# Optimization experiments

Measured on AMD Instinct MI355X. Metric: run time of the kernel, lower is better.

## Reference

```python
import jax, jax.numpy as jnp
import numpy as np


def setup_inputs() -> dict:
    key = jax.random.key(0)
    k1, k2, k3 = jax.random.split(key, 3)
    B, Cin, Cout, L, K = 16, 64, 64, 65536, 3
    return {
        "x": jax.random.normal(k1, (B, Cin, L), dtype=jnp.float32),
        "alpha": jnp.zeros((1, Cin, 1), dtype=jnp.float32),
        "weight": jax.random.normal(k2, (Cout, Cin, K), dtype=jnp.float32),
        "weight_scale": jnp.ones((Cout, 1, 1), dtype=jnp.float32),
        "bias": jax.random.normal(k3, (Cout,), dtype=jnp.float32),
        "beta": jnp.ones((1, Cout, 1), dtype=jnp.float32),
        "gamma": jnp.zeros((1, Cout, 1), dtype=jnp.float32),
        "zeta": jnp.zeros((1, Cout, 1), dtype=jnp.float32),
    }


def _rsign(x, alpha):
    # forward: sign(x - alpha) in {-1,+1}; backward: identity w.r.t. x (STE)
    signed = jnp.where(x >= alpha, 1.0, -1.0).astype(x.dtype)
    return x + jax.lax.stop_gradient(signed - x)


def _clipped_ste_sign(w):
    # forward: sign(w); backward: grad passes only where |w| <= 1 (Bi-RealNet)
    w_bin = jnp.sign(w)
    mask = (jnp.abs(w) <= 1.0).astype(w.dtype)
    wm = w * mask
    return jax.lax.stop_gradient(w_bin) + wm - jax.lax.stop_gradient(wm)


def _rprelu(x, beta, gamma, zeta):
    xs = x - gamma
    return jnp.where(x > gamma, xs + zeta, beta * xs + zeta)


def reference(x, alpha, weight, weight_scale, bias, beta, gamma, zeta):
    # RSign -> scaled binary conv1d (stride=1, pad=1) -> RPReLU
    xb = _rsign(x, alpha)                        # [B,Cin,L], values +-1
    wb = _clipped_ste_sign(weight) * weight_scale  # [Cout,Cin,K]
    y = jax.lax.conv_general_dilated(
        xb, wb, window_strides=(1,), padding=[(1, 1)],
        dimension_numbers=("NCH", "OIH", "NCH"))  # [B,Cout,L]
    y = y + bias[None, :, None]
    return _rprelu(y, beta, gamma, zeta)
```

## Files before the change

kernel.cpp:

```cpp
#include <hip/hip_runtime.h>

#define LLEN 65536
#define CIN 64
#define COUT 64
#define BROW (LLEN + 8)

typedef float f32x4 __attribute__((ext_vector_type(4)));
typedef unsigned long long u64;
typedef u64 u64x4 __attribute__((ext_vector_type(4)));

struct __align__(64) WRec {
    u64 p0, p1, p2;
    float A;
    float S;
    float Bv, G, Z;
    float f0, f2;
    float pad[3];
};

__global__ void pack_weights(const float* __restrict__ w,
                             const float* __restrict__ wscale,
                             const float* __restrict__ bias,
                             const float* __restrict__ beta,
                             const float* __restrict__ gamma,
                             const float* __restrict__ zeta,
                             WRec* __restrict__ rec) {
    int co = threadIdx.x;
    if (co >= COUT) return;
    const float* wr = w + co * (CIN * 3);
    u64 p[3] = {0, 0, 0}, nzw[3] = {0, 0, 0};
    #pragma unroll
    for (int q = 0; q < 4; ++q) {
        f32x4 buf[12];
        #pragma unroll
        for (int j = 0; j < 12; ++j)
            buf[j] = *(const f32x4*)(wr + q * 48 + 4 * j);
        #pragma unroll
        for (int j = 0; j < 12; ++j) {
            #pragma unroll
            for (int m = 0; m < 4; ++m) {
                const int idx = q * 48 + 4 * j + m;
                const int ci = idx / 3, k = idx % 3;
                const float wv = buf[j][m];
                p[k]   |= ((u64)(wv > 0.0f)) << ci;
                nzw[k] |= ((u64)(wv != 0.0f)) << ci;
            }
        }
    }
    const int n0 = __popcll(nzw[0]), n1 = __popcll(nzw[1]), n2 = __popcll(nzw[2]);
    WRec r;
    float s = wscale[co];
    r.p0 = p[0]; r.p1 = p[1]; r.p2 = p[2];
    r.A  = s * (float)(n0 + n1 + n2) + bias[co];
    r.S  = -2.0f * s;
    r.Bv = beta[co]; r.G = gamma[co]; r.Z = zeta[co];
    r.f0 = 0.5f * (float)n0;
    r.f2 = 0.5f * (float)n2;
    r.pad[0] = r.pad[1] = r.pad[2] = 0.0f;
    rec[co] = r;
}

__global__ void __launch_bounds__(256) pack_x(
        const float* __restrict__ x,
        const float* __restrict__ alpha,
        u64* __restrict__ bits) {
    const int t = threadIdx.x;
    const int b = blockIdx.y;
    const int l0 = blockIdx.x * 1024 + 4 * t;
    const float* xb = x + (size_t)b * CIN * LLEN + l0;

    u64 w0 = 0, w1 = 0, w2 = 0, w3 = 0;
    #pragma unroll
    for (int q = 0; q < 8; ++q) {
        f32x4 buf[8];
        #pragma unroll
        for (int j = 0; j < 8; ++j)
            buf[j] = *(const f32x4*)(xb + (size_t)(q * 8 + j) * LLEN);
        #pragma unroll
        for (int j = 0; j < 8; ++j) {
            const int ci = q * 8 + j;
            const float a = alpha[ci];
            w0 |= ((u64)(buf[j].x >= a)) << ci;
            w1 |= ((u64)(buf[j].y >= a)) << ci;
            w2 |= ((u64)(buf[j].z >= a)) << ci;
            w3 |= ((u64)(buf[j].w >= a)) << ci;
        }
    }
    u64x4 v; v.x = w0; v.y = w1; v.z = w2; v.w = w3;
    *(u64x4*)(bits + (size_t)b * BROW + l0 + 4) = v;
}

__device__ __forceinline__ float rprelu(float y, float B, float G, float Z) {
    float xs = y - G;
    return (y > G) ? (xs + Z) : fmaf(B, xs, Z);
}

__global__ void __launch_bounds__(256) bconv_compute(
        const u64* __restrict__ bits,
        const WRec* __restrict__ rec,
        float* __restrict__ out) {
    const int t     = threadIdx.x;
    const int co    = blockIdx.x;
    const int chunk = blockIdx.y;
    const int b     = blockIdx.z;
    const int c0    = chunk * 8192;

    const WRec r = rec[co];
    const u64* base = bits + (size_t)b * BROW + c0 + 4 * t;
    float* outp = out + ((size_t)b * COUT + co) * LLEN + c0 + 4 * t;

    const bool lo = (chunk == 0) && (t == 0);
    const bool hi = (chunk == 7) && (t == 255);

    #pragma unroll 4
    for (int j = 0; j < 8; ++j) {
        const u64* src = base + 1024 * j;
        const u64 xq0 = src[3], xq1 = src[4], xq2 = src[5],
                  xq3 = src[6], xq4 = src[7], xq5 = src[8];

        float fx = (float)(__popcll(xq0 ^ r.p0) + __popcll(xq1 ^ r.p1)
                         + __popcll(xq2 ^ r.p2));
        float fy = (float)(__popcll(xq1 ^ r.p0) + __popcll(xq2 ^ r.p1)
                         + __popcll(xq3 ^ r.p2));
        float fz = (float)(__popcll(xq2 ^ r.p0) + __popcll(xq3 ^ r.p1)
                         + __popcll(xq4 ^ r.p2));
        float fw = (float)(__popcll(xq3 ^ r.p0) + __popcll(xq4 ^ r.p1)
                         + __popcll(xq5 ^ r.p2));
        if (j == 0 && lo)
            fx = (float)(__popcll(xq1 ^ r.p1) + __popcll(xq2 ^ r.p2)) + r.f0;
        if (j == 7 && hi)
            fw = (float)(__popcll(xq3 ^ r.p0) + __popcll(xq4 ^ r.p1)) + r.f2;

        f32x4 o;
        o.x = rprelu(fmaf(r.S, fx, r.A), r.Bv, r.G, r.Z);
        o.y = rprelu(fmaf(r.S, fy, r.A), r.Bv, r.G, r.Z);
        o.z = rprelu(fmaf(r.S, fz, r.A), r.Bv, r.G, r.Z);
        o.w = rprelu(fmaf(r.S, fw, r.A), r.Bv, r.G, r.Z);
        __builtin_nontemporal_store(o, (f32x4*)(outp + 1024 * j));
    }
}

extern "C" void kernel_launch(void* const* d_in, const int* in_sizes, int n_in,
                              void* d_out, int out_size, void* d_ws, size_t ws_size,
                              hipStream_t stream) {
    const float* x      = (const float*)d_in[0];
    const float* alpha  = (const float*)d_in[1];
    const float* w      = (const float*)d_in[2];
    const float* wscale = (const float*)d_in[3];
    const float* bias   = (const float*)d_in[4];
    const float* beta   = (const float*)d_in[5];
    const float* gamma  = (const float*)d_in[6];
    const float* zeta   = (const float*)d_in[7];
    float* out = (float*)d_out;

    WRec* rec = (WRec*)d_ws;
    u64* bits = (u64*)((char*)d_ws + 4096);

    pack_weights<<<1, 64, 0, stream>>>(w, wscale, bias, beta, gamma, zeta, rec);

    dim3 gridA(LLEN / 1024, 16);
    pack_x<<<gridA, 256, 0, stream>>>(x, alpha, bits);

    dim3 gridB(COUT, 8, 16);
    bconv_compute<<<gridB, 256, 0, stream>>>(bits, rec, out);
}
```

Before: 103.6 us.

## Fold weight packing into pack_x, double per-thread work, swap compute grid order

Removes the separate one-block weight-packing launch by running it from an extra column of blocks in pack_x. Each pack_x thread now handles two 4-element groups with nontemporal loads, halving the block count and raising memory-level parallelism. The compute grid now has the chunk as the fastest block index instead of the output channel, which changes which blocks run concurrently and how bit-packed input rows are reused in cache. Risks include higher register pressure in pack_x and worse L2 reuse of the packed bits across output channels.

```diff
diff --git a/kernel.cpp b/kernel.cpp
--- a/kernel.cpp
+++ b/kernel.cpp
@@ -4,6 +4,7 @@
 #define CIN 64
 #define COUT 64
 #define BROW (LLEN + 8)
+#define NBLK_A (LLEN / 2048)
 
 typedef float f32x4 __attribute__((ext_vector_type(4)));
 typedef unsigned long long u64;
@@ -18,13 +19,11 @@
     float pad[3];
 };
 
-__global__ void pack_weights(const float* __restrict__ w,
-                             const float* __restrict__ wscale,
-                             const float* __restrict__ bias,
-                             const float* __restrict__ beta,
-                             const float* __restrict__ gamma,
-                             const float* __restrict__ zeta,
-                             WRec* __restrict__ rec) {
+__device__ __forceinline__ void pack_weights_body(
+        const float* __restrict__ w, const float* __restrict__ wscale,
+        const float* __restrict__ bias, const float* __restrict__ beta,
+        const float* __restrict__ gamma, const float* __restrict__ zeta,
+        WRec* __restrict__ rec) {
     int co = threadIdx.x;
     if (co >= COUT) return;
     const float* wr = w + co * (CIN * 3);
@@ -63,31 +62,54 @@
 __global__ void __launch_bounds__(256) pack_x(
         const float* __restrict__ x,
         const float* __restrict__ alpha,
-        u64* __restrict__ bits) {
+        u64* __restrict__ bits,
+        const float* __restrict__ w,
+        const float* __restrict__ wscale,
+        const float* __restrict__ bias,
+        const float* __restrict__ beta,
+        const float* __restrict__ gamma,
+        const float* __restrict__ zeta,
+        WRec* __restrict__ rec) {
+    if (blockIdx.x == NBLK_A) {
+        if (blockIdx.y == 0)
+            pack_weights_body(w, wscale, bias, beta, gamma, zeta, rec);
+        return;
+    }
     const int t = threadIdx.x;
     const int b = blockIdx.y;
-    const int l0 = blockIdx.x * 1024 + 4 * t;
-    const float* xb = x + (size_t)b * CIN * LLEN + l0;
+    const int l0 = blockIdx.x * 2048;
+    const float* xb = x + (size_t)b * CIN * LLEN + l0 + 4 * t;
 
-    u64 w0 = 0, w1 = 0, w2 = 0, w3 = 0;
+    u64 wa0 = 0, wa1 = 0, wa2 = 0, wa3 = 0;
+    u64 wb0 = 0, wb1 = 0, wb2 = 0, wb3 = 0;
     #pragma unroll
-    for (int q = 0; q < 8; ++q) {
-        f32x4 buf[8];
+    for (int q = 0; q < 16; ++q) {
+        f32x4 blo[4], bhi[4];
         #pragma unroll
-        for (int j = 0; j < 8; ++j)
-            buf[j] = *(const f32x4*)(xb + (size_t)(q * 8 + j) * LLEN);
+        for (int j = 0; j < 4; ++j) {
+            const float* rp = xb + (size_t)(q * 4 + j) * LLEN;
+            blo[j] = __builtin_nontemporal_load((const f32x4*)rp);
+            bhi[j] = __builtin_nontemporal_load((const f32x4*)(rp + 1024));
+        }
         #pragma unroll
-        for (int j = 0; j < 8; ++j) {
-            const int ci = q * 8 + j;
+        for (int j = 0; j < 4; ++j) {
+            const int ci = q * 4 + j;
             const float a = alpha[ci];
-            w0 |= ((u64)(buf[j].x >= a)) << ci;
-            w1 |= ((u64)(buf[j].y >= a)) << ci;
-            w2 |= ((u64)(buf[j].z >= a)) << ci;
-            w3 |= ((u64)(buf[j].w >= a)) << ci;
+            wa0 |= ((u64)(blo[j].x >= a)) << ci;
+            wa1 |= ((u64)(blo[j].y >= a)) << ci;
+            wa2 |= ((u64)(blo[j].z >= a)) << ci;
+            wa3 |= ((u64)(blo[j].w >= a)) << ci;
+            wb0 |= ((u64)(bhi[j].x >= a)) << ci;
+            wb1 |= ((u64)(bhi[j].y >= a)) << ci;
+            wb2 |= ((u64)(bhi[j].z >= a)) << ci;
+            wb3 |= ((u64)(bhi[j].w >= a)) << ci;
         }
     }
-    u64x4 v; v.x = w0; v.y = w1; v.z = w2; v.w = w3;
-    *(u64x4*)(bits + (size_t)b * BROW + l0 + 4) = v;
+    u64* dst = bits + (size_t)b * BROW + l0 + 4 * t + 4;
+    u64x4 va; va.x = wa0; va.y = wa1; va.z = wa2; va.w = wa3;
+    u64x4 vb; vb.x = wb0; vb.y = wb1; vb.z = wb2; vb.w = wb3;
+    *(u64x4*)dst = va;
+    *(u64x4*)(dst + 1024) = vb;
 }
 
 __device__ __forceinline__ float rprelu(float y, float B, float G, float Z) {
@@ -100,8 +122,8 @@
         const WRec* __restrict__ rec,
         float* __restrict__ out) {
     const int t     = threadIdx.x;
-    const int co    = blockIdx.x;
-    const int chunk = blockIdx.y;
+    const int chunk = blockIdx.x;
+    const int co    = blockIdx.y;
     const int b     = blockIdx.z;
     const int c0    = chunk * 8192;
 
@@ -156,11 +178,10 @@
     WRec* rec = (WRec*)d_ws;
     u64* bits = (u64*)((char*)d_ws + 4096);
 
-    pack_weights<<<1, 64, 0, stream>>>(w, wscale, bias, beta, gamma, zeta, rec);
+    dim3 gridA(NBLK_A + 1, 16);
+    pack_x<<<gridA, 256, 0, stream>>>(x, alpha, bits, w, wscale, bias,
+                                      beta, gamma, zeta, rec);
 
-    dim3 gridA(LLEN / 1024, 16);
-    pack_x<<<gridA, 256, 0, stream>>>(x, alpha, bits);
-
-    dim3 gridB(COUT, 8, 16);
+    dim3 gridB(8, COUT, 16);
     bconv_compute<<<gridB, 256, 0, stream>>>(bits, rec, out);
 }
```

Result: no change. 102.7 us, median of 2 (-0.8%).
